# Kernel optimization log

Hardware: AMD Instinct MI355X
Metric: run time of the kernel (lower is better)

## Reference

```python
import jax, jax.numpy as jnp
import numpy as np

B, T, H, L = 8, 2048, 256, 16


def setup_inputs() -> dict:
    key = jax.random.key(0)
    ks = jax.random.split(key, 6)
    return {
        "logits": jax.random.normal(ks[0], (B, T, H), dtype=jnp.float32),
        "end_w": jax.random.normal(ks[1], (H,), dtype=jnp.float32),      # end_fc weight (no bias)
        "whole_w": jax.random.normal(ks[2], (L, H), dtype=jnp.float32),
        "relay_w": jax.random.normal(ks[3], (H,), dtype=jnp.float32),    # relay_fc weight
        "relay_b": jax.random.normal(ks[4], (), dtype=jnp.float32),      # relay_fc bias
        "length_bias": jax.random.normal(ks[5], (L,), dtype=jnp.float32),
    }


def reference(logits, end_w, whole_w, relay_w, relay_b, length_bias):
    # logits: [B, T, H]
    Lh, Hh = whole_w.shape
    Tt = logits.shape[1]
    # left-pad with L-1 zero frames: start_logits[b,t,l] = logits[b, t-l] (zeros if t-l < 0)
    pad = jnp.pad(logits, ((0, 0), (Lh - 1, 0), (0, 0)))  # [B, T+L-1, H]
    start_logits = jnp.stack(
        [pad[:, Lh - 1 - l: Lh - 1 - l + Tt, :] for l in range(Lh)], axis=2
    )  # [B, T, L, H]
    # elementwise max of current-position logits against each window start
    logits_max = jnp.maximum(logits[:, :, None, :], start_logits)  # [B, T, L, H]
    whole_scores = jnp.einsum('btlh,lh->btl', logits_max, whole_w)  # [B, T, L]
    end_scores = jnp.einsum('bth,h->bt', logits, end_w)[:, :, None]  # [B, T, 1]
    # relay branch: shift logits left by L (zero-pad tail), elementwise max with logits
    relay_tmp = jnp.pad(logits[:, Lh:, :], ((0, 0), (0, Lh), (0, 0)))  # [B, T, H]
    relay_logits_max = jnp.maximum(relay_tmp, logits)
    relay_scores = jnp.einsum('bth,h->bt', relay_logits_max, relay_w) + relay_b  # [B, T]
    out = whole_scores + end_scores + length_bias[None, None, :]
    return out, relay_scores
```

## Files before the change

### kernel.cpp

```cpp
#include <hip/hip_runtime.h>

#define BB 8
#define TT 2048
#define HH 256
#define LL 16

__global__ __launch_bounds__(256) void ffm_kernel(
    const float* __restrict__ logits,
    const float* __restrict__ end_w,
    const float* __restrict__ whole_w,
    const float* __restrict__ relay_w,
    const float* __restrict__ relay_b,
    const float* __restrict__ length_bias,
    float* __restrict__ out)
{
    const int tid  = threadIdx.x;
    const int lane = tid & 63;
    const int wv   = tid >> 6;
    const int bid  = blockIdx.x;
    const int b    = bid & 7;
    const int t    = ((bid >> 3) << 2) + wv;

    const float4* lg4 = (const float4*)logits;
    const int rowbase = (b * TT + t) * (HH / 4) + lane;

    const float4 cur = lg4[rowbase];

    float4 ww[LL];
#pragma unroll
    for (int l = 0; l < LL; ++l)
        ww[l] = ((const float4*)whole_w)[l * (HH / 4) + lane];
    const float4 ew = ((const float4*)end_w)[lane];
    const float4 rw = ((const float4*)relay_w)[lane];

    float vals[18];

    vals[0] = cur.x * ww[0].x + cur.y * ww[0].y + cur.z * ww[0].z + cur.w * ww[0].w;

#pragma unroll
    for (int l = 1; l < LL; ++l) {
        float4 row = make_float4(0.f, 0.f, 0.f, 0.f);
        if (t >= l) row = lg4[rowbase - l * (HH / 4)];
        const float mx = fmaxf(cur.x, row.x);
        const float my = fmaxf(cur.y, row.y);
        const float mz = fmaxf(cur.z, row.z);
        const float mw = fmaxf(cur.w, row.w);
        vals[l] = mx * ww[l].x + my * ww[l].y + mz * ww[l].z + mw * ww[l].w;
    }

    vals[16] = cur.x * ew.x + cur.y * ew.y + cur.z * ew.z + cur.w * ew.w;

    {
        float4 rr = make_float4(0.f, 0.f, 0.f, 0.f);
        if (t + LL < TT) rr = lg4[rowbase + LL * (HH / 4)];
        const float mx = fmaxf(cur.x, rr.x);
        const float my = fmaxf(cur.y, rr.y);
        const float mz = fmaxf(cur.z, rr.z);
        const float mw = fmaxf(cur.w, rr.w);
        vals[17] = mx * rw.x + my * rw.y + mz * rw.z + mw * rw.w;
    }

#pragma unroll
    for (int v = 0; v < 18; ++v) {
        float s = vals[v];
        s += __shfl_xor(s, 32);
        s += __shfl_xor(s, 16);
        s += __shfl_xor(s, 8);
        s += __shfl_xor(s, 4);
        s += __shfl_xor(s, 2);
        s += __shfl_xor(s, 1);
        vals[v] = s;
    }

    if (lane == 0) {
        const float ev = vals[16];
        float4* op = (float4*)(out + (size_t)(b * TT + t) * LL);
#pragma unroll
        for (int q = 0; q < 4; ++q) {
            float4 o;
            o.x = vals[q * 4 + 0] + ev + length_bias[q * 4 + 0];
            o.y = vals[q * 4 + 1] + ev + length_bias[q * 4 + 1];
            o.z = vals[q * 4 + 2] + ev + length_bias[q * 4 + 2];
            o.w = vals[q * 4 + 3] + ev + length_bias[q * 4 + 3];
            op[q] = o;
        }
        out[(size_t)BB * TT * LL + b * TT + t] = vals[17] + relay_b[0];
    }
}

extern "C" void kernel_launch(void* const* d_in, const int* in_sizes, int n_in,
                              void* d_out, int out_size, void* d_ws, size_t ws_size,
                              hipStream_t stream) {
    const float* logits  = (const float*)d_in[0];
    const float* end_w   = (const float*)d_in[1];
    const float* whole_w = (const float*)d_in[2];
    const float* relay_w = (const float*)d_in[3];
    const float* relay_b = (const float*)d_in[4];
    const float* lbias   = (const float*)d_in[5];
    float* out = (float*)d_out;

    dim3 grid(BB * TT / 4);
    dim3 block(256);
    hipLaunchKernelGGL(ffm_kernel, grid, block, 0, stream,
                       logits, end_w, whole_w, relay_w, relay_b, lbias, out);
}
```

Measured before the change: 96.72 us.

## Process eight timesteps per wave with register row reuse and DPP reductions

Each wave now handles eight consecutive timesteps and loads the 23 needed logits rows into registers once. This replaces up to 16 separate global loads per timestep, removing most redundant load traffic. Wave reductions switch from shfl_xor to DPP row/bcast operations, with the result read from lane 63. The length bias and relay bias are hoisted into registers and the grid shrinks to match. The cost is much higher register pressure from 23 float4 rows plus 16 weight float4s, which may reduce occupancy or cause spills.

```diff
diff --git a/kernel.cpp b/kernel.cpp
--- a/kernel.cpp
+++ b/kernel.cpp
@@ -4,8 +4,32 @@
 #define TT 2048
 #define HH 256
 #define LL 16
+#define SS 8
+#define NR (LL - 1 + SS)
 
-__global__ __launch_bounds__(256) void ffm_kernel(
+__device__ __forceinline__ float wave_sum_lane63(float v) {
+    int x;
+    x = __builtin_amdgcn_update_dpp(0, __float_as_int(v), 0x111, 0xf, 0xf, true);
+    v += __int_as_float(x);
+    x = __builtin_amdgcn_update_dpp(0, __float_as_int(v), 0x112, 0xf, 0xf, true);
+    v += __int_as_float(x);
+    x = __builtin_amdgcn_update_dpp(0, __float_as_int(v), 0x114, 0xf, 0xf, true);
+    v += __int_as_float(x);
+    x = __builtin_amdgcn_update_dpp(0, __float_as_int(v), 0x118, 0xf, 0xf, true);
+    v += __int_as_float(x);
+    x = __builtin_amdgcn_update_dpp(0, __float_as_int(v), 0x142, 0xa, 0xf, true);
+    v += __int_as_float(x);
+    x = __builtin_amdgcn_update_dpp(0, __float_as_int(v), 0x143, 0xc, 0xf, true);
+    v += __int_as_float(x);
+    return v;
+}
+
+__device__ __forceinline__ float dotmax4(const float4 a, const float4 p, const float4 w) {
+    return fmaxf(a.x, p.x) * w.x + fmaxf(a.y, p.y) * w.y +
+           fmaxf(a.z, p.z) * w.z + fmaxf(a.w, p.w) * w.w;
+}
+
+__global__ __launch_bounds__(256, 2) void ffm_kernel(
     const float* __restrict__ logits,
     const float* __restrict__ end_w,
     const float* __restrict__ whole_w,
@@ -14,77 +38,76 @@
     const float* __restrict__ length_bias,
     float* __restrict__ out)
 {
-    const int tid  = threadIdx.x;
-    const int lane = tid & 63;
-    const int wv   = tid >> 6;
-    const int bid  = blockIdx.x;
-    const int b    = bid & 7;
-    const int t    = ((bid >> 3) << 2) + wv;
+    const int tid   = threadIdx.x;
+    const int lane  = tid & 63;
+    const int wv    = tid >> 6;
+    const int bid   = blockIdx.x;
+    const int b     = bid & 7;
+    const int tbase = ((bid >> 3) * 4 + wv) * SS;
 
     const float4* lg4 = (const float4*)logits;
-    const int rowbase = (b * TT + t) * (HH / 4) + lane;
+    const long rowstr = HH / 4;
+    const long base   = (long)(b * TT) * rowstr + lane;
 
-    const float4 cur = lg4[rowbase];
+    const float4 z4 = make_float4(0.f, 0.f, 0.f, 0.f);
 
     float4 ww[LL];
 #pragma unroll
     for (int l = 0; l < LL; ++l)
-        ww[l] = ((const float4*)whole_w)[l * (HH / 4) + lane];
+        ww[l] = ((const float4*)whole_w)[l * rowstr + lane];
     const float4 ew = ((const float4*)end_w)[lane];
     const float4 rw = ((const float4*)relay_w)[lane];
 
-    float vals[18];
+    float lb[LL];
+#pragma unroll
+    for (int q = 0; q < 4; ++q) {
+        const float4 l4 = ((const float4*)length_bias)[q];
+        lb[4 * q + 0] = l4.x; lb[4 * q + 1] = l4.y;
+        lb[4 * q + 2] = l4.z; lb[4 * q + 3] = l4.w;
+    }
+    const float rb = relay_b[0];
 
-    vals[0] = cur.x * ww[0].x + cur.y * ww[0].y + cur.z * ww[0].z + cur.w * ww[0].w;
-
+    float4 rows[NR];
 #pragma unroll
-    for (int l = 1; l < LL; ++l) {
-        float4 row = make_float4(0.f, 0.f, 0.f, 0.f);
-        if (t >= l) row = lg4[rowbase - l * (HH / 4)];
-        const float mx = fmaxf(cur.x, row.x);
-        const float my = fmaxf(cur.y, row.y);
-        const float mz = fmaxf(cur.z, row.z);
-        const float mw = fmaxf(cur.w, row.w);
-        vals[l] = mx * ww[l].x + my * ww[l].y + mz * ww[l].z + mw * ww[l].w;
-    }
-
-    vals[16] = cur.x * ew.x + cur.y * ew.y + cur.z * ew.z + cur.w * ew.w;
-
-    {
-        float4 rr = make_float4(0.f, 0.f, 0.f, 0.f);
-        if (t + LL < TT) rr = lg4[rowbase + LL * (HH / 4)];
-        const float mx = fmaxf(cur.x, rr.x);
-        const float my = fmaxf(cur.y, rr.y);
-        const float mz = fmaxf(cur.z, rr.z);
-        const float mw = fmaxf(cur.w, rr.w);
-        vals[17] = mx * rw.x + my * rw.y + mz * rw.z + mw * rw.w;
+    for (int i = 0; i < NR; ++i) {
+        const int r = tbase - (LL - 1) + i;
+        rows[i] = (r >= 0) ? lg4[base + (long)r * rowstr] : z4;
     }
 
 #pragma unroll
-    for (int v = 0; v < 18; ++v) {
-        float s = vals[v];
-        s += __shfl_xor(s, 32);
-        s += __shfl_xor(s, 16);
-        s += __shfl_xor(s, 8);
-        s += __shfl_xor(s, 4);
-        s += __shfl_xor(s, 2);
-        s += __shfl_xor(s, 1);
-        vals[v] = s;
-    }
+    for (int s = 0; s < SS; ++s) {
+        const int t = tbase + s;
+        const float4 cur = rows[LL - 1 + s];
 
-    if (lane == 0) {
-        const float ev = vals[16];
-        float4* op = (float4*)(out + (size_t)(b * TT + t) * LL);
+        float vals[18];
 #pragma unroll
-        for (int q = 0; q < 4; ++q) {
-            float4 o;
-            o.x = vals[q * 4 + 0] + ev + length_bias[q * 4 + 0];
-            o.y = vals[q * 4 + 1] + ev + length_bias[q * 4 + 1];
-            o.z = vals[q * 4 + 2] + ev + length_bias[q * 4 + 2];
-            o.w = vals[q * 4 + 3] + ev + length_bias[q * 4 + 3];
-            op[q] = o;
+        for (int l = 0; l < LL; ++l)
+            vals[l] = dotmax4(cur, rows[LL - 1 + s - l], ww[l]);
+
+        vals[16] = cur.x * ew.x + cur.y * ew.y + cur.z * ew.z + cur.w * ew.w;
+
+        float4 rr = z4;
+        if (t + LL < TT) rr = lg4[base + (long)(t + LL) * rowstr];
+        vals[17] = dotmax4(cur, rr, rw);
+
+#pragma unroll
+        for (int v = 0; v < 18; ++v)
+            vals[v] = wave_sum_lane63(vals[v]);
+
+        if (lane == 63) {
+            const float ev = vals[16];
+            float4* op = (float4*)(out + (size_t)(b * TT + t) * LL);
+#pragma unroll
+            for (int q = 0; q < 4; ++q) {
+                float4 o;
+                o.x = vals[4 * q + 0] + ev + lb[4 * q + 0];
+                o.y = vals[4 * q + 1] + ev + lb[4 * q + 1];
+                o.z = vals[4 * q + 2] + ev + lb[4 * q + 2];
+                o.w = vals[4 * q + 3] + ev + lb[4 * q + 3];
+                op[q] = o;
+            }
+            out[(size_t)BB * TT * LL + (size_t)(b * TT + t)] = vals[17] + rb;
         }
-        out[(size_t)BB * TT * LL + b * TT + t] = vals[17] + relay_b[0];
     }
 }
 
@@ -99,7 +122,7 @@
     const float* lbias   = (const float*)d_in[5];
     float* out = (float*)d_out;
 
-    dim3 grid(BB * TT / 4);
+    dim3 grid(BB * TT / (SS * 4));
     dim3 block(256);
     hipLaunchKernelGGL(ffm_kernel, grid, block, 0, stream,
                        logits, end_w, whole_w, relay_w, relay_b, lbias, out);
```

Result: faster. 90.74 us (-6.2%).
